# Optimization experiments

Hardware: AMD Instinct MI355X
Metric: run time of the kernel (lower is better)

The kernel has to match this reference:

```python
import jax, jax.numpy as jnp
import numpy as np

EMBED = 1024
HEADS = 16

def setup_inputs() -> dict:
    key = jax.random.key(0)
    ks = jax.random.split(key, 6)
    N, S = 1, 4096
    half = EMBED // 2
    x = jax.random.normal(ks[0], (N, S, EMBED), dtype=jnp.float32)
    Wq = jax.random.normal(ks[1], (half, half), dtype=jnp.float32) * 0.02
    Wk = jax.random.normal(ks[2], (half, half), dtype=jnp.float32) * 0.02
    Wv = jax.random.normal(ks[3], (half, half), dtype=jnp.float32) * 0.02
    Wo = jax.random.normal(ks[4], (EMBED, half), dtype=jnp.float32) * 0.02
    bo = jnp.zeros((EMBED,), dtype=jnp.float32)
    return {"x": x, "Wq": Wq, "Wk": Wk, "Wv": Wv, "Wo": Wo, "bo": bo}

def reference(x, Wq, Wk, Wv, Wo, bo):
    N, S, E = x.shape
    H = HEADS
    Dh = (E // 2) // H                 # per-head dim of the half-width projections (32)
    scale = float(E // H) ** 0.5       # original scales by head_dim = embed/heads = 64
    left = x[..., : E // 2]            # only the left chunk feeds attention in the source
    # torch Linear: y = x @ W.T (no bias)
    q = (left @ Wq.T).reshape(N, S, H, Dh)
    k = (left @ Wk.T).reshape(N, S, H, Dh)
    v = (left @ Wv.T).reshape(N, S, H, Dh)
    energy = jnp.einsum('nqhd,nkhd->nqkh', q, k)          # [N,S,S,H] full score tensor
    att = jax.nn.softmax(energy / scale, axis=2)          # softmax over key axis
    out = jnp.einsum('nqkh,nkhd->nqhd', att, v)           # [N,S,H,Dh]
    out = out.reshape(N, S, E // 2)
    return out @ Wo.T + bo                                # fc_out: half -> embed
```

## Files before the change

### kernel.cpp

```cpp
#include <hip/hip_runtime.h>
#include <stdint.h>


#define SEQ    4096
#define DMODEL 1024
#define DHALF  512
#define NH     16
#define DH     32
#define NSPLIT 2
#define KSPAN  (SEQ / NSPLIT)

typedef __attribute__((ext_vector_type(4))) float facc4;
typedef __attribute__((ext_vector_type(8))) short bfrag8;

#define MFMA_BF16(a, b, c) __builtin_amdgcn_mfma_f32_16x16x32_bf16((a), (b), (c), 0, 0, 0)

static __device__ __forceinline__ uint16_t f2b(float x) {
    uint32_t u = __float_as_uint(x);
    return (uint16_t)((u + 0x7FFFu + ((u >> 16) & 1u)) >> 16);
}
static __device__ __forceinline__ float b2f(uint16_t b) {
    return __uint_as_float(((uint32_t)b) << 16);
}

static __device__ __forceinline__ bfrag8 cvt8(const float* __restrict__ s) {
    float4 a = *(const float4*)s;
    float4 b = *(const float4*)(s + 4);
    bfrag8 r;
    r[0] = (short)f2b(a.x); r[1] = (short)f2b(a.y);
    r[2] = (short)f2b(a.z); r[3] = (short)f2b(a.w);
    r[4] = (short)f2b(b.x); r[5] = (short)f2b(b.y);
    r[6] = (short)f2b(b.z); r[7] = (short)f2b(b.w);
    return r;
}

__global__ __launch_bounds__(256) void convert_all(
    const float* __restrict__ x,  const float* __restrict__ Wq,
    const float* __restrict__ Wk, const float* __restrict__ Wv,
    const float* __restrict__ Wo,
    uint16_t* __restrict__ xbf, uint16_t* __restrict__ Wqb,
    uint16_t* __restrict__ Wkb, uint16_t* __restrict__ Wvb,
    uint16_t* __restrict__ Wob)
{
    int bid = blockIdx.x;
    if (bid < 1024) {
        int t   = bid * 256 + threadIdx.x;
        int row = t >> 6;
        int cb  = (t & 63) << 3;
        *(bfrag8*)&xbf[(size_t)row * DHALF + cb] = cvt8(&x[(size_t)row * DMODEL + cb]);
    } else {
        int zz = bid - 1024;
        const float* src; uint16_t* dst; size_t off;
        if      (zz < 128) { src = Wq; dst = Wqb; off = (size_t)zz * 2048; }
        else if (zz < 256) { src = Wk; dst = Wkb; off = (size_t)(zz - 128) * 2048; }
        else if (zz < 384) { src = Wv; dst = Wvb; off = (size_t)(zz - 256) * 2048; }
        else               { src = Wo; dst = Wob; off = (size_t)(zz - 384) * 2048; }
        size_t i = off + (size_t)threadIdx.x * 8;
        *(bfrag8*)&dst[i] = cvt8(&src[i]);
    }
}

__device__ __forceinline__ void gemm128(
    const uint16_t* __restrict__ A, int lda,
    const uint16_t* __restrict__ B, int ldb,
    void* __restrict__ C, int ldc, int cF32,
    const float* __restrict__ bias, float scale,
    int Kd, int m0, int n0)
{
    __shared__ __align__(16) uint16_t As[2][128 * 40];
    __shared__ __align__(16) uint16_t Bs[2][128 * 40];

    const int tid  = threadIdx.x;
    const int lane = tid & 63;
    const int wv   = tid >> 6;
    const int lo   = lane & 15;
    const int quad = lane >> 4;
    const int srow = tid >> 2;
    const int skq  = (tid & 3) * 8;
    const int rb   = (wv >> 1) * 64;
    const int cb   = (wv & 1) * 64;

    const facc4 ZACC = {0.f, 0.f, 0.f, 0.f};
    facc4 acc[4][4];
#pragma unroll
    for (int i = 0; i < 4; ++i)
#pragma unroll
        for (int j = 0; j < 4; ++j) acc[i][j] = ZACC;

    const uint16_t* pA0 = &A[(size_t)(m0 + srow) * lda + skq];
    const uint16_t* pA1 = &A[(size_t)(m0 + srow + 64) * lda + skq];
    const uint16_t* pB0 = &B[(size_t)(n0 + srow) * ldb + skq];
    const uint16_t* pB1 = &B[(size_t)(n0 + srow + 64) * ldb + skq];

    bfrag8 ra0 = *(const bfrag8*)pA0;
    bfrag8 ra1 = *(const bfrag8*)pA1;
    bfrag8 rb0 = *(const bfrag8*)pB0;
    bfrag8 rb1 = *(const bfrag8*)pB1;

    *(bfrag8*)&As[0][srow * 40 + skq]        = ra0;
    *(bfrag8*)&As[0][(srow + 64) * 40 + skq] = ra1;
    *(bfrag8*)&Bs[0][srow * 40 + skq]        = rb0;
    *(bfrag8*)&Bs[0][(srow + 64) * 40 + skq] = rb1;
    __syncthreads();

    int p = 0;
    for (int kt = 0; kt < Kd; kt += 32) {
        const bool more = (kt + 32 < Kd);
        if (more) {
            ra0 = *(const bfrag8*)(pA0 + kt + 32);
            ra1 = *(const bfrag8*)(pA1 + kt + 32);
            rb0 = *(const bfrag8*)(pB0 + kt + 32);
            rb1 = *(const bfrag8*)(pB1 + kt + 32);
        }

        bfrag8 af[4], bf[4];
#pragma unroll
        for (int i = 0; i < 4; ++i) {
            af[i] = *(const bfrag8*)&As[p][(rb + i * 16 + lo) * 40 + quad * 8];
            bf[i] = *(const bfrag8*)&Bs[p][(cb + i * 16 + lo) * 40 + quad * 8];
        }
#pragma unroll
        for (int i = 0; i < 4; ++i)
#pragma unroll
            for (int j = 0; j < 4; ++j)
                acc[i][j] = MFMA_BF16(af[i], bf[j], acc[i][j]);

        if (more) {
            *(bfrag8*)&As[1 - p][srow * 40 + skq]        = ra0;
            *(bfrag8*)&As[1 - p][(srow + 64) * 40 + skq] = ra1;
            *(bfrag8*)&Bs[1 - p][srow * 40 + skq]        = rb0;
            *(bfrag8*)&Bs[1 - p][(srow + 64) * 40 + skq] = rb1;
            __syncthreads();
            p ^= 1;
        }
    }

#pragma unroll
    for (int j = 0; j < 4; ++j) {
        int col  = n0 + cb + j * 16 + lo;
        float bv = bias ? bias[col] : 0.f;
#pragma unroll
        for (int i = 0; i < 4; ++i) {
#pragma unroll
            for (int r = 0; r < 4; ++r) {
                int row = m0 + rb + i * 16 + quad * 4 + r;
                float v = acc[i][j][r] * scale + bv;
                if (cF32) ((float*)C)[(size_t)row * ldc + col] = v;
                else      ((uint16_t*)C)[(size_t)row * ldc + col] = f2b(v);
            }
        }
    }
}

#define SC_Q (0.125f * 1.4426950408889634f)

__global__ __launch_bounds__(256, 2) void qkv_kernel(
    const uint16_t* __restrict__ xbf,
    const uint16_t* __restrict__ Wqb, const uint16_t* __restrict__ Wkb,
    const uint16_t* __restrict__ Wvb,
    uint16_t* __restrict__ Q, uint16_t* __restrict__ K, uint16_t* __restrict__ V)
{
    const int z = blockIdx.z;
    const uint16_t* W = (z == 0) ? Wqb : (z == 1) ? Wkb : Wvb;
    uint16_t* Out     = (z == 0) ? Q   : (z == 1) ? K   : V;
    float scale       = (z == 0) ? SC_Q : 1.0f;
    gemm128(xbf, DHALF, W, DHALF, Out, DHALF, 0, nullptr, scale, DHALF,
            blockIdx.y * 128, blockIdx.x * 128);
}

__global__ __launch_bounds__(256, 2) void outproj_kernel(
    const uint16_t* __restrict__ O, const uint16_t* __restrict__ Wob,
    const float* __restrict__ bo, float* __restrict__ Y)
{
    gemm128(O, DHALF, Wob, DHALF, Y, DMODEL, 1, bo, 1.0f, DHALF,
            blockIdx.y * 128, blockIdx.x * 128);
}

__global__ __launch_bounds__(256) void attn_kernel(
    const uint16_t* __restrict__ Q, const uint16_t* __restrict__ Kb,
    const uint16_t* __restrict__ Vb, uint16_t* __restrict__ Op,
    float* __restrict__ lbuf)
{
    __shared__ __align__(16) uint16_t Ks[2][64 * 40];
    __shared__ __align__(16) uint16_t Vt[2][32 * 64];
    __shared__ __align__(16) uint16_t Ps[4 * 16 * 72];

    const int tid  = threadIdx.x;
    const int lane = tid & 63;
    const int wv   = tid >> 6;
    const int lo   = lane & 15;
    const int quad = lane >> 4;
    const int h    = blockIdx.y;
    const int q0   = blockIdx.x * 64;
    const int sp   = blockIdx.z;
    const int srow = tid >> 2;
    const int skq  = (tid & 3) * 8;

    const facc4 ZACC = {0.f, 0.f, 0.f, 0.f};

    const bfrag8 qf = *(const bfrag8*)&Q[(size_t)(q0 + wv * 16 + lo) * DHALF + h * DH + quad * 8];

    int vt_w[8];
#pragma unroll
    for (int j = 0; j < 8; ++j) {
        int d  = skq + j;
        int Rd = ((d & 7) + 2 * (d >> 3)) & 7;
        vt_w[j] = d * 64 + ((((srow >> 3) + Rd) & 7) << 3) + (srow & 7);
    }
    int vt_r[2][2];
#pragma unroll
    for (int dt = 0; dt < 2; ++dt) {
        int d  = dt * 16 + lo;
        int Rd = ((d & 7) + 2 * (d >> 3)) & 7;
#pragma unroll
        for (int c = 0; c < 2; ++c)
            vt_r[c][dt] = d * 64 + ((((c * 4 + quad) + Rd) & 7) << 3);
    }
    const int pbase = wv * (16 * 72);
    const int ps_w  = pbase + lo * 72 + 4 * quad;
    const int ps_r  = pbase + lo * 72 + quad * 8;
    const int ks_r  = lo * 40 + quad * 8;

    const uint16_t* pK = &Kb[(size_t)srow * DHALF + h * DH + skq];
    const uint16_t* pV = &Vb[(size_t)srow * DHALF + h * DH + skq];

    facc4 oacc[2];
    oacc[0] = ZACC; oacc[1] = ZACC;
    float lpart = 0.f;

    const int kb0  = sp * KSPAN;
    const int kend = kb0 + KSPAN;

    float4 kreg = *(const float4*)(pK + (size_t)kb0 * DHALF);
    float4 vreg = *(const float4*)(pV + (size_t)kb0 * DHALF);

    *(float4*)&Ks[0][srow * 40 + skq] = kreg;
    {
        const uint16_t* vp = (const uint16_t*)&vreg;
#pragma unroll
        for (int j = 0; j < 8; ++j) Vt[0][vt_w[j]] = vp[j];
    }
    __syncthreads();

    int p = 0;
    for (int kb = kb0; kb < kend; kb += 64) {
        const bool more = (kb + 64 < kend);
        if (more) {
            kreg = *(const float4*)(pK + (size_t)(kb + 64) * DHALF);
            vreg = *(const float4*)(pV + (size_t)(kb + 64) * DHALF);
        }

#pragma unroll
        for (int t = 0; t < 4; ++t) {
            bfrag8 kf = *(const bfrag8*)&Ks[p][t * 640 + ks_r];
            facc4 s = MFMA_BF16(kf, qf, ZACC);
            float p0 = __builtin_amdgcn_exp2f(s[0]);
            float p1 = __builtin_amdgcn_exp2f(s[1]);
            float p2 = __builtin_amdgcn_exp2f(s[2]);
            float p3 = __builtin_amdgcn_exp2f(s[3]);
            lpart += (p0 + p1) + (p2 + p3);
            uint32_t u0 = __float_as_uint(p0) + 0x8000u;
            uint32_t u1 = __float_as_uint(p1) + 0x8000u;
            uint32_t u2 = __float_as_uint(p2) + 0x8000u;
            uint32_t u3 = __float_as_uint(p3) + 0x8000u;
            uint2 w;
            w.x = __builtin_amdgcn_perm(u1, u0, 0x07060302u);
            w.y = __builtin_amdgcn_perm(u3, u2, 0x07060302u);
            *(uint2*)&Ps[ps_w + 16 * t] = w;
        }
        __builtin_amdgcn_wave_barrier();

#pragma unroll
        for (int c = 0; c < 2; ++c) {
            bfrag8 pf = *(const bfrag8*)&Ps[ps_r + c * 32];
#pragma unroll
            for (int dt = 0; dt < 2; ++dt) {
                bfrag8 vf = *(const bfrag8*)&Vt[p][vt_r[c][dt]];
                oacc[dt] = MFMA_BF16(pf, vf, oacc[dt]);
            }
        }

        if (more) {
            *(float4*)&Ks[1 - p][srow * 40 + skq] = kreg;
            const uint16_t* vp = (const uint16_t*)&vreg;
#pragma unroll
            for (int j = 0; j < 8; ++j) Vt[1 - p][vt_w[j]] = vp[j];
            __syncthreads();
            p ^= 1;
        }
    }

    float lfull = lpart;
    lfull += __shfl_xor(lfull, 16);
    lfull += __shfl_xor(lfull, 32);
    if (quad == 0)
        lbuf[((size_t)sp * NH + h) * SEQ + q0 + wv * 16 + lo] = lfull;

    uint16_t* Od = Op + (size_t)sp * SEQ * DHALF;
#pragma unroll
    for (int r = 0; r < 4; ++r) {
        int row = q0 + wv * 16 + quad * 4 + r;
        Od[(size_t)row * DHALF + h * DH + lo]      = f2b(oacc[0][r]);
        Od[(size_t)row * DHALF + h * DH + 16 + lo] = f2b(oacc[1][r]);
    }
}

__global__ __launch_bounds__(256) void combine_kernel(
    const uint16_t* __restrict__ Op, const float* __restrict__ lbuf,
    uint16_t* __restrict__ O)
{
    int t   = blockIdx.x * 256 + threadIdx.x;
    int row = t >> 6;
    int cb  = (t & 63) << 3;
    int h   = cb >> 5;
    float inv = 1.0f / (lbuf[(size_t)h * SEQ + row] +
                        lbuf[((size_t)NH + h) * SEQ + row]);
    const uint16_t* p0 = &Op[(size_t)row * DHALF + cb];
    const uint16_t* p1 = p0 + (size_t)SEQ * DHALF;
    bfrag8 a = *(const bfrag8*)p0;
    bfrag8 b = *(const bfrag8*)p1;
    bfrag8 o;
#pragma unroll
    for (int j = 0; j < 8; ++j)
        o[j] = (short)f2b((b2f((uint16_t)a[j]) + b2f((uint16_t)b[j])) * inv);
    *(bfrag8*)&O[(size_t)row * DHALF + cb] = o;
}

extern "C" void kernel_launch(void* const* d_in, const int* in_sizes, int n_in,
                              void* d_out, int out_size, void* d_ws, size_t ws_size,
                              hipStream_t stream)
{
    const float* x  = (const float*)d_in[0];
    const float* Wq = (const float*)d_in[1];
    const float* Wk = (const float*)d_in[2];
    const float* Wv = (const float*)d_in[3];
    const float* Wo = (const float*)d_in[4];
    const float* bo = (const float*)d_in[5];

    uint16_t* xbf = (uint16_t*)d_ws;
    uint16_t* Wqb = xbf + (size_t)SEQ * DHALF;
    uint16_t* Wkb = Wqb + (size_t)DHALF * DHALF;
    uint16_t* Wvb = Wkb + (size_t)DHALF * DHALF;
    uint16_t* Wob = Wvb + (size_t)DHALF * DHALF;
    uint16_t* Q   = Wob + (size_t)DMODEL * DHALF;
    uint16_t* K   = Q + (size_t)SEQ * DHALF;
    uint16_t* V   = K + (size_t)SEQ * DHALF;
    uint16_t* O   = V + (size_t)SEQ * DHALF;
    uint16_t* Op  = O + (size_t)SEQ * DHALF;
    float*  lbuf  = (float*)(Op + (size_t)NSPLIT * SEQ * DHALF);

    convert_all<<<1664, 256, 0, stream>>>(x, Wq, Wk, Wv, Wo, xbf, Wqb, Wkb, Wvb, Wob);
    qkv_kernel<<<dim3(DHALF / 128, SEQ / 128, 3), 256, 0, stream>>>(
        xbf, Wqb, Wkb, Wvb, Q, K, V);
    attn_kernel<<<dim3(SEQ / 64, NH, NSPLIT), 256, 0, stream>>>(Q, K, V, Op, lbuf);
    combine_kernel<<<1024, 256, 0, stream>>>(Op, lbuf, O);
    outproj_kernel<<<dim3(DMODEL / 128, SEQ / 128), 256, 0, stream>>>(
        O, Wob, bo, (float*)d_out);
}
```

Baseline: 197.7 us.

## Split attention keys across waves and keep P in registers via K16 MFMA

```diff
diff --git a/kernel.cpp b/kernel.cpp
--- a/kernel.cpp
+++ b/kernel.cpp
@@ -12,8 +12,10 @@
 
 typedef __attribute__((ext_vector_type(4))) float facc4;
 typedef __attribute__((ext_vector_type(8))) short bfrag8;
-
-#define MFMA_BF16(a, b, c) __builtin_amdgcn_mfma_f32_16x16x32_bf16((a), (b), (c), 0, 0, 0)
+typedef __attribute__((ext_vector_type(4))) short bpack4;
+
+#define MFMA_BF16(a, b, c)  __builtin_amdgcn_mfma_f32_16x16x32_bf16((a), (b), (c), 0, 0, 0)
+#define MFMA_BF16_K16(a, b, c) __builtin_amdgcn_mfma_f32_16x16x16bf16_1k((a), (b), (c), 0, 0, 0)
 
 static __device__ __forceinline__ uint16_t f2b(float x) {
     uint32_t u = __float_as_uint(x);
@@ -181,9 +183,9 @@
     const uint16_t* __restrict__ Vb, uint16_t* __restrict__ Op,
     float* __restrict__ lbuf)
 {
-    __shared__ __align__(16) uint16_t Ks[2][64 * 40];
     __shared__ __align__(16) uint16_t Vt[2][32 * 64];
-    __shared__ __align__(16) uint16_t Ps[4 * 16 * 72];
+    __shared__ float Ored[64][33];
+    __shared__ float lsh[4][64];
 
     const int tid  = threadIdx.x;
     const int lane = tid & 63;
@@ -198,7 +200,10 @@
 
     const facc4 ZACC = {0.f, 0.f, 0.f, 0.f};
 
-    const bfrag8 qf = *(const bfrag8*)&Q[(size_t)(q0 + wv * 16 + lo) * DHALF + h * DH + quad * 8];
+    bfrag8 qf[4];
+#pragma unroll
+    for (int t = 0; t < 4; ++t)
+        qf[t] = *(const bfrag8*)&Q[(size_t)(q0 + t * 16 + lo) * DHALF + h * DH + quad * 8];
 
     int vt_w[8];
 #pragma unroll
@@ -207,34 +212,28 @@
         int Rd = ((d & 7) + 2 * (d >> 3)) & 7;
         vt_w[j] = d * 64 + ((((srow >> 3) + Rd) & 7) << 3) + (srow & 7);
     }
-    int vt_r[2][2];
+    int vt_r[2];
 #pragma unroll
     for (int dt = 0; dt < 2; ++dt) {
         int d  = dt * 16 + lo;
         int Rd = ((d & 7) + 2 * (d >> 3)) & 7;
-#pragma unroll
-        for (int c = 0; c < 2; ++c)
-            vt_r[c][dt] = d * 64 + ((((c * 4 + quad) + Rd) & 7) << 3);
-    }
-    const int pbase = wv * (16 * 72);
-    const int ps_w  = pbase + lo * 72 + 4 * quad;
-    const int ps_r  = pbase + lo * 72 + quad * 8;
-    const int ks_r  = lo * 40 + quad * 8;
-
-    const uint16_t* pK = &Kb[(size_t)srow * DHALF + h * DH + skq];
+        vt_r[dt] = d * 64 + ((((2 * wv + (quad >> 1)) + Rd) & 7) << 3) + (quad & 1) * 4;
+    }
+
+    const uint16_t* pK = &Kb[(size_t)(wv * 16 + lo) * DHALF + h * DH + quad * 8];
     const uint16_t* pV = &Vb[(size_t)srow * DHALF + h * DH + skq];
 
-    facc4 oacc[2];
-    oacc[0] = ZACC; oacc[1] = ZACC;
-    float lpart = 0.f;
+    facc4 oacc[4][2];
+#pragma unroll
+    for (int t = 0; t < 4; ++t) { oacc[t][0] = ZACC; oacc[t][1] = ZACC; }
+    float lp[4] = {0.f, 0.f, 0.f, 0.f};
 
     const int kb0  = sp * KSPAN;
     const int kend = kb0 + KSPAN;
 
-    float4 kreg = *(const float4*)(pK + (size_t)kb0 * DHALF);
+    bfrag8 kf   = *(const bfrag8*)(pK + (size_t)kb0 * DHALF);
     float4 vreg = *(const float4*)(pV + (size_t)kb0 * DHALF);
 
-    *(float4*)&Ks[0][srow * 40 + skq] = kreg;
     {
         const uint16_t* vp = (const uint16_t*)&vreg;
 #pragma unroll
@@ -245,20 +244,24 @@
     int p = 0;
     for (int kb = kb0; kb < kend; kb += 64) {
         const bool more = (kb + 64 < kend);
+        bfrag8 kf2;
         if (more) {
-            kreg = *(const float4*)(pK + (size_t)(kb + 64) * DHALF);
+            kf2  = *(const bfrag8*)(pK + (size_t)(kb + 64) * DHALF);
             vreg = *(const float4*)(pV + (size_t)(kb + 64) * DHALF);
         }
 
+        bpack4 vf[2];
+        vf[0] = *(const bpack4*)&Vt[p][vt_r[0]];
+        vf[1] = *(const bpack4*)&Vt[p][vt_r[1]];
+
 #pragma unroll
         for (int t = 0; t < 4; ++t) {
-            bfrag8 kf = *(const bfrag8*)&Ks[p][t * 640 + ks_r];
-            facc4 s = MFMA_BF16(kf, qf, ZACC);
+            facc4 s = MFMA_BF16(kf, qf[t], ZACC);
             float p0 = __builtin_amdgcn_exp2f(s[0]);
             float p1 = __builtin_amdgcn_exp2f(s[1]);
             float p2 = __builtin_amdgcn_exp2f(s[2]);
             float p3 = __builtin_amdgcn_exp2f(s[3]);
-            lpart += (p0 + p1) + (p2 + p3);
+            lp[t] += (p0 + p1) + (p2 + p3);
             uint32_t u0 = __float_as_uint(p0) + 0x8000u;
             uint32_t u1 = __float_as_uint(p1) + 0x8000u;
             uint32_t u2 = __float_as_uint(p2) + 0x8000u;
@@ -266,42 +269,58 @@
             uint2 w;
             w.x = __builtin_amdgcn_perm(u1, u0, 0x07060302u);
             w.y = __builtin_amdgcn_perm(u3, u2, 0x07060302u);
-            *(uint2*)&Ps[ps_w + 16 * t] = w;
-        }
-        __builtin_amdgcn_wave_barrier();
-
-#pragma unroll
-        for (int c = 0; c < 2; ++c) {
-            bfrag8 pf = *(const bfrag8*)&Ps[ps_r + c * 32];
-#pragma unroll
-            for (int dt = 0; dt < 2; ++dt) {
-                bfrag8 vf = *(const bfrag8*)&Vt[p][vt_r[c][dt]];
-                oacc[dt] = MFMA_BF16(pf, vf, oacc[dt]);
-            }
+            bpack4 pf = *(bpack4*)&w;
+#pragma unroll
+            for (int dt = 0; dt < 2; ++dt)
+                oacc[t][dt] = MFMA_BF16_K16(pf, vf[dt], oacc[t][dt]);
         }
 
         if (more) {
-            *(float4*)&Ks[1 - p][srow * 40 + skq] = kreg;
             const uint16_t* vp = (const uint16_t*)&vreg;
 #pragma unroll
             for (int j = 0; j < 8; ++j) Vt[1 - p][vt_w[j]] = vp[j];
+            kf = kf2;
             __syncthreads();
             p ^= 1;
         }
     }
 
-    float lfull = lpart;
-    lfull += __shfl_xor(lfull, 16);
-    lfull += __shfl_xor(lfull, 32);
-    if (quad == 0)
-        lbuf[((size_t)sp * NH + h) * SEQ + q0 + wv * 16 + lo] = lfull;
-
-    uint16_t* Od = Op + (size_t)sp * SEQ * DHALF;
-#pragma unroll
-    for (int r = 0; r < 4; ++r) {
-        int row = q0 + wv * 16 + quad * 4 + r;
-        Od[(size_t)row * DHALF + h * DH + lo]      = f2b(oacc[0][r]);
-        Od[(size_t)row * DHALF + h * DH + 16 + lo] = f2b(oacc[1][r]);
+#pragma unroll
+    for (int t = 0; t < 4; ++t) {
+        float l = lp[t];
+        l += __shfl_xor(l, 16);
+        l += __shfl_xor(l, 32);
+        if (quad == 0) lsh[wv][t * 16 + lo] = l;
+    }
+
+    for (int w = 0; w < 4; ++w) {
+        if (wv == w) {
+#pragma unroll
+            for (int t = 0; t < 4; ++t)
+#pragma unroll
+                for (int dt = 0; dt < 2; ++dt)
+#pragma unroll
+                    for (int r = 0; r < 4; ++r) {
+                        int q = t * 16 + quad * 4 + r;
+                        int d = dt * 16 + lo;
+                        if (w == 0) Ored[q][d]  = oacc[t][dt][r];
+                        else        Ored[q][d] += oacc[t][dt][r];
+                    }
+        }
+        __syncthreads();
+    }
+
+    {
+        int row = tid >> 2;
+        int dc  = (tid & 3) * 8;
+        bfrag8 o8;
+#pragma unroll
+        for (int j = 0; j < 8; ++j) o8[j] = (short)f2b(Ored[row][dc + j]);
+        uint16_t* Od = Op + (size_t)sp * SEQ * DHALF;
+        *(bfrag8*)&Od[(size_t)(q0 + row) * DHALF + h * DH + dc] = o8;
+        if (tid < 64)
+            lbuf[((size_t)sp * NH + h) * SEQ + q0 + tid] =
+                lsh[0][tid] + lsh[1][tid] + lsh[2][tid] + lsh[3][tid];
     }
 }
 
```

Result: slower. 213.6 us (+8.0%).

## Fuse x conversion into QKV GEMM, single-buffer attention, compute rowsum via MFMA

Applied to the files above, without the earlier changes.

```diff
diff --git a/kernel.cpp b/kernel.cpp
--- a/kernel.cpp
+++ b/kernel.cpp
@@ -7,8 +7,6 @@
 #define DHALF  512
 #define NH     16
 #define DH     32
-#define NSPLIT 2
-#define KSPAN  (SEQ / NSPLIT)
 
 typedef __attribute__((ext_vector_type(4))) float facc4;
 typedef __attribute__((ext_vector_type(8))) short bfrag8;
@@ -23,45 +21,40 @@
     return __uint_as_float(((uint32_t)b) << 16);
 }
 
-static __device__ __forceinline__ bfrag8 cvt8(const float* __restrict__ s) {
-    float4 a = *(const float4*)s;
-    float4 b = *(const float4*)(s + 4);
-    bfrag8 r;
-    r[0] = (short)f2b(a.x); r[1] = (short)f2b(a.y);
-    r[2] = (short)f2b(a.z); r[3] = (short)f2b(a.w);
-    r[4] = (short)f2b(b.x); r[5] = (short)f2b(b.y);
-    r[6] = (short)f2b(b.z); r[7] = (short)f2b(b.w);
-    return r;
-}
-
-__global__ __launch_bounds__(256) void convert_all(
-    const float* __restrict__ x,  const float* __restrict__ Wq,
-    const float* __restrict__ Wk, const float* __restrict__ Wv,
-    const float* __restrict__ Wo,
-    uint16_t* __restrict__ xbf, uint16_t* __restrict__ Wqb,
-    uint16_t* __restrict__ Wkb, uint16_t* __restrict__ Wvb,
-    uint16_t* __restrict__ Wob)
-{
-    int bid = blockIdx.x;
-    if (bid < 1024) {
-        int t   = bid * 256 + threadIdx.x;
-        int row = t >> 6;
-        int cb  = (t & 63) << 3;
-        *(bfrag8*)&xbf[(size_t)row * DHALF + cb] = cvt8(&x[(size_t)row * DMODEL + cb]);
-    } else {
-        int zz = bid - 1024;
-        const float* src; uint16_t* dst; size_t off;
-        if      (zz < 128) { src = Wq; dst = Wqb; off = (size_t)zz * 2048; }
-        else if (zz < 256) { src = Wk; dst = Wkb; off = (size_t)(zz - 128) * 2048; }
-        else if (zz < 384) { src = Wv; dst = Wvb; off = (size_t)(zz - 256) * 2048; }
-        else               { src = Wo; dst = Wob; off = (size_t)(zz - 384) * 2048; }
-        size_t i = off + (size_t)threadIdx.x * 8;
-        *(bfrag8*)&dst[i] = cvt8(&src[i]);
-    }
-}
-
-__device__ __forceinline__ void gemm128(
-    const uint16_t* __restrict__ A, int lda,
+static __device__ __forceinline__ bfrag8 cvt8perm(float4 a, float4 b) {
+    uint32_t u0 = __float_as_uint(a.x) + 0x8000u, u1 = __float_as_uint(a.y) + 0x8000u;
+    uint32_t u2 = __float_as_uint(a.z) + 0x8000u, u3 = __float_as_uint(a.w) + 0x8000u;
+    uint32_t u4 = __float_as_uint(b.x) + 0x8000u, u5 = __float_as_uint(b.y) + 0x8000u;
+    uint32_t u6 = __float_as_uint(b.z) + 0x8000u, u7 = __float_as_uint(b.w) + 0x8000u;
+    union { uint32_t w[4]; bfrag8 r; } u;
+    u.w[0] = __builtin_amdgcn_perm(u1, u0, 0x07060302u);
+    u.w[1] = __builtin_amdgcn_perm(u3, u2, 0x07060302u);
+    u.w[2] = __builtin_amdgcn_perm(u5, u4, 0x07060302u);
+    u.w[3] = __builtin_amdgcn_perm(u7, u6, 0x07060302u);
+    return u.r;
+}
+
+__global__ __launch_bounds__(256) void convert_w(
+    const float* __restrict__ Wq, const float* __restrict__ Wk,
+    const float* __restrict__ Wv, const float* __restrict__ Wo,
+    uint16_t* __restrict__ q, uint16_t* __restrict__ k,
+    uint16_t* __restrict__ v, uint16_t* __restrict__ o)
+{
+    int zz = blockIdx.x;
+    const float* src; uint16_t* dst; size_t off;
+    if      (zz < 128) { src = Wq; dst = q; off = (size_t)zz * 2048; }
+    else if (zz < 256) { src = Wk; dst = k; off = (size_t)(zz - 128) * 2048; }
+    else if (zz < 384) { src = Wv; dst = v; off = (size_t)(zz - 256) * 2048; }
+    else               { src = Wo; dst = o; off = (size_t)(zz - 384) * 2048; }
+    size_t i = off + (size_t)threadIdx.x * 8;
+    float4 a = *(const float4*)&src[i];
+    float4 b = *(const float4*)&src[i + 4];
+    *(bfrag8*)&dst[i] = cvt8perm(a, b);
+}
+
+template <int AF32>
+__device__ __forceinline__ void gemm128T(
+    const void* __restrict__ A, int lda,
     const uint16_t* __restrict__ B, int ldb,
     void* __restrict__ C, int ldc, int cF32,
     const float* __restrict__ bias, float scale,
@@ -87,18 +80,32 @@
 #pragma unroll
         for (int j = 0; j < 4; ++j) acc[i][j] = ZACC;
 
-    const uint16_t* pA0 = &A[(size_t)(m0 + srow) * lda + skq];
-    const uint16_t* pA1 = &A[(size_t)(m0 + srow + 64) * lda + skq];
+    const float*    fA0 = AF32 ? &((const float*)A)[(size_t)(m0 + srow) * lda + skq] : nullptr;
+    const float*    fA1 = AF32 ? &((const float*)A)[(size_t)(m0 + srow + 64) * lda + skq] : nullptr;
+    const uint16_t* hA0 = AF32 ? nullptr : &((const uint16_t*)A)[(size_t)(m0 + srow) * lda + skq];
+    const uint16_t* hA1 = AF32 ? nullptr : &((const uint16_t*)A)[(size_t)(m0 + srow + 64) * lda + skq];
     const uint16_t* pB0 = &B[(size_t)(n0 + srow) * ldb + skq];
     const uint16_t* pB1 = &B[(size_t)(n0 + srow + 64) * ldb + skq];
 
-    bfrag8 ra0 = *(const bfrag8*)pA0;
-    bfrag8 ra1 = *(const bfrag8*)pA1;
+    bfrag8 ra0, ra1;
+    float4 f0a, f0b, f1a, f1b;
+    if (AF32) {
+        f0a = *(const float4*)fA0; f0b = *(const float4*)(fA0 + 4);
+        f1a = *(const float4*)fA1; f1b = *(const float4*)(fA1 + 4);
+    } else {
+        ra0 = *(const bfrag8*)hA0;
+        ra1 = *(const bfrag8*)hA1;
+    }
     bfrag8 rb0 = *(const bfrag8*)pB0;
     bfrag8 rb1 = *(const bfrag8*)pB1;
 
-    *(bfrag8*)&As[0][srow * 40 + skq]        = ra0;
-    *(bfrag8*)&As[0][(srow + 64) * 40 + skq] = ra1;
+    if (AF32) {
+        *(bfrag8*)&As[0][srow * 40 + skq]        = cvt8perm(f0a, f0b);
+        *(bfrag8*)&As[0][(srow + 64) * 40 + skq] = cvt8perm(f1a, f1b);
+    } else {
+        *(bfrag8*)&As[0][srow * 40 + skq]        = ra0;
+        *(bfrag8*)&As[0][(srow + 64) * 40 + skq] = ra1;
+    }
     *(bfrag8*)&Bs[0][srow * 40 + skq]        = rb0;
     *(bfrag8*)&Bs[0][(srow + 64) * 40 + skq] = rb1;
     __syncthreads();
@@ -107,8 +114,13 @@
     for (int kt = 0; kt < Kd; kt += 32) {
         const bool more = (kt + 32 < Kd);
         if (more) {
-            ra0 = *(const bfrag8*)(pA0 + kt + 32);
-            ra1 = *(const bfrag8*)(pA1 + kt + 32);
+            if (AF32) {
+                f0a = *(const float4*)(fA0 + kt + 32); f0b = *(const float4*)(fA0 + kt + 36);
+                f1a = *(const float4*)(fA1 + kt + 32); f1b = *(const float4*)(fA1 + kt + 36);
+            } else {
+                ra0 = *(const bfrag8*)(hA0 + kt + 32);
+                ra1 = *(const bfrag8*)(hA1 + kt + 32);
+            }
             rb0 = *(const bfrag8*)(pB0 + kt + 32);
             rb1 = *(const bfrag8*)(pB1 + kt + 32);
         }
@@ -126,8 +138,13 @@
                 acc[i][j] = MFMA_BF16(af[i], bf[j], acc[i][j]);
 
         if (more) {
-            *(bfrag8*)&As[1 - p][srow * 40 + skq]        = ra0;
-            *(bfrag8*)&As[1 - p][(srow + 64) * 40 + skq] = ra1;
+            if (AF32) {
+                *(bfrag8*)&As[1 - p][srow * 40 + skq]        = cvt8perm(f0a, f0b);
+                *(bfrag8*)&As[1 - p][(srow + 64) * 40 + skq] = cvt8perm(f1a, f1b);
+            } else {
+                *(bfrag8*)&As[1 - p][srow * 40 + skq]        = ra0;
+                *(bfrag8*)&As[1 - p][(srow + 64) * 40 + skq] = ra1;
+            }
             *(bfrag8*)&Bs[1 - p][srow * 40 + skq]        = rb0;
             *(bfrag8*)&Bs[1 - p][(srow + 64) * 40 + skq] = rb1;
             __syncthreads();
@@ -155,7 +172,7 @@
 #define SC_Q (0.125f * 1.4426950408889634f)
 
 __global__ __launch_bounds__(256, 2) void qkv_kernel(
-    const uint16_t* __restrict__ xbf,
+    const float* __restrict__ x,
     const uint16_t* __restrict__ Wqb, const uint16_t* __restrict__ Wkb,
     const uint16_t* __restrict__ Wvb,
     uint16_t* __restrict__ Q, uint16_t* __restrict__ K, uint16_t* __restrict__ V)
@@ -164,25 +181,25 @@
     const uint16_t* W = (z == 0) ? Wqb : (z == 1) ? Wkb : Wvb;
     uint16_t* Out     = (z == 0) ? Q   : (z == 1) ? K   : V;
     float scale       = (z == 0) ? SC_Q : 1.0f;
-    gemm128(xbf, DHALF, W, DHALF, Out, DHALF, 0, nullptr, scale, DHALF,
-            blockIdx.y * 128, blockIdx.x * 128);
+    gemm128T<1>(x, DMODEL, W, DHALF, Out, DHALF, 0, nullptr, scale, DHALF,
+                blockIdx.y * 128, blockIdx.x * 128);
 }
 
 __global__ __launch_bounds__(256, 2) void outproj_kernel(
     const uint16_t* __restrict__ O, const uint16_t* __restrict__ Wob,
     const float* __restrict__ bo, float* __restrict__ Y)
 {
-    gemm128(O, DHALF, Wob, DHALF, Y, DMODEL, 1, bo, 1.0f, DHALF,
-            blockIdx.y * 128, blockIdx.x * 128);
+    gemm128T<0>(O, DHALF, Wob, DHALF, Y, DMODEL, 1, bo, 1.0f, DHALF,
+                blockIdx.y * 128, blockIdx.x * 128);
 }
 
 __global__ __launch_bounds__(256) void attn_kernel(
     const uint16_t* __restrict__ Q, const uint16_t* __restrict__ Kb,
     const uint16_t* __restrict__ Vb, uint16_t* __restrict__ Op,
-    float* __restrict__ lbuf)
-{
-    __shared__ __align__(16) uint16_t Ks[2][64 * 40];
-    __shared__ __align__(16) uint16_t Vt[2][32 * 64];
+    float* __restrict__ lbuf, int kspan)
+{
+    __shared__ __align__(16) uint16_t Ks[64 * 40];
+    __shared__ __align__(16) uint16_t Vt[32 * 64];
     __shared__ __align__(16) uint16_t Ps[4 * 16 * 72];
 
     const int tid  = threadIdx.x;
@@ -200,6 +217,10 @@
 
     const bfrag8 qf = *(const bfrag8*)&Q[(size_t)(q0 + wv * 16 + lo) * DHALF + h * DH + quad * 8];
 
+    bfrag8 ones;
+#pragma unroll
+    for (int j = 0; j < 8; ++j) ones[j] = (short)0x3F80;
+
     int vt_w[8];
 #pragma unroll
     for (int j = 0; j < 8; ++j) {
@@ -224,41 +245,37 @@
     const uint16_t* pK = &Kb[(size_t)srow * DHALF + h * DH + skq];
     const uint16_t* pV = &Vb[(size_t)srow * DHALF + h * DH + skq];
 
-    facc4 oacc[2];
-    oacc[0] = ZACC; oacc[1] = ZACC;
-    float lpart = 0.f;
-
-    const int kb0  = sp * KSPAN;
-    const int kend = kb0 + KSPAN;
+    facc4 oacc[2], oaccL;
+    oacc[0] = ZACC; oacc[1] = ZACC; oaccL = ZACC;
+
+    const int kb0  = sp * kspan;
+    const int kend = kb0 + kspan;
 
     float4 kreg = *(const float4*)(pK + (size_t)kb0 * DHALF);
     float4 vreg = *(const float4*)(pV + (size_t)kb0 * DHALF);
 
-    *(float4*)&Ks[0][srow * 40 + skq] = kreg;
-    {
-        const uint16_t* vp = (const uint16_t*)&vreg;
-#pragma unroll
-        for (int j = 0; j < 8; ++j) Vt[0][vt_w[j]] = vp[j];
-    }
-    __syncthreads();
-
-    int p = 0;
     for (int kb = kb0; kb < kend; kb += 64) {
-        const bool more = (kb + 64 < kend);
-        if (more) {
+        *(float4*)&Ks[srow * 40 + skq] = kreg;
+        {
+            const uint16_t* vp = (const uint16_t*)&vreg;
+#pragma unroll
+            for (int j = 0; j < 8; ++j) Vt[vt_w[j]] = vp[j];
+        }
+        __syncthreads();
+
+        if (kb + 64 < kend) {
             kreg = *(const float4*)(pK + (size_t)(kb + 64) * DHALF);
             vreg = *(const float4*)(pV + (size_t)(kb + 64) * DHALF);
         }
 
 #pragma unroll
         for (int t = 0; t < 4; ++t) {
-            bfrag8 kf = *(const bfrag8*)&Ks[p][t * 640 + ks_r];
+            bfrag8 kf = *(const bfrag8*)&Ks[t * 640 + ks_r];
             facc4 s = MFMA_BF16(kf, qf, ZACC);
             float p0 = __builtin_amdgcn_exp2f(s[0]);
             float p1 = __builtin_amdgcn_exp2f(s[1]);
             float p2 = __builtin_amdgcn_exp2f(s[2]);
             float p3 = __builtin_amdgcn_exp2f(s[3]);
-            lpart += (p0 + p1) + (p2 + p3);
             uint32_t u0 = __float_as_uint(p0) + 0x8000u;
             uint32_t u1 = __float_as_uint(p1) + 0x8000u;
             uint32_t u2 = __float_as_uint(p2) + 0x8000u;
@@ -275,26 +292,19 @@
             bfrag8 pf = *(const bfrag8*)&Ps[ps_r + c * 32];
 #pragma unroll
             for (int dt = 0; dt < 2; ++dt) {
-                bfrag8 vf = *(const bfrag8*)&Vt[p][vt_r[c][dt]];
+                bfrag8 vf = *(const bfrag8*)&Vt[vt_r[c][dt]];
                 oacc[dt] = MFMA_BF16(pf, vf, oacc[dt]);
             }
-        }
-
-        if (more) {
-            *(float4*)&Ks[1 - p][srow * 40 + skq] = kreg;
-            const uint16_t* vp = (const uint16_t*)&vreg;
-#pragma unroll
-            for (int j = 0; j < 8; ++j) Vt[1 - p][vt_w[j]] = vp[j];
-            __syncthreads();
-            p ^= 1;
-        }
-    }
-
-    float lfull = lpart;
-    lfull += __shfl_xor(lfull, 16);
-    lfull += __shfl_xor(lfull, 32);
-    if (quad == 0)
-        lbuf[((size_t)sp * NH + h) * SEQ + q0 + wv * 16 + lo] = lfull;
+            oaccL = MFMA_BF16(pf, ones, oaccL);
+        }
+        __syncthreads();
+    }
+
+    if (lo == 0) {
+#pragma unroll
+        for (int r = 0; r < 4; ++r)
+            lbuf[((size_t)sp * NH + h) * SEQ + q0 + wv * 16 + quad * 4 + r] = oaccL[r];
+    }
 
     uint16_t* Od = Op + (size_t)sp * SEQ * DHALF;
 #pragma unroll
@@ -307,22 +317,24 @@
 
 __global__ __launch_bounds__(256) void combine_kernel(
     const uint16_t* __restrict__ Op, const float* __restrict__ lbuf,
-    uint16_t* __restrict__ O)
+    uint16_t* __restrict__ O, int ns)
 {
     int t   = blockIdx.x * 256 + threadIdx.x;
     int row = t >> 6;
     int cb  = (t & 63) << 3;
     int h   = cb >> 5;
-    float inv = 1.0f / (lbuf[(size_t)h * SEQ + row] +
-                        lbuf[((size_t)NH + h) * SEQ + row]);
-    const uint16_t* p0 = &Op[(size_t)row * DHALF + cb];
-    const uint16_t* p1 = p0 + (size_t)SEQ * DHALF;
-    bfrag8 a = *(const bfrag8*)p0;
-    bfrag8 b = *(const bfrag8*)p1;
+    float l = 0.f;
+    float acc[8] = {0.f, 0.f, 0.f, 0.f, 0.f, 0.f, 0.f, 0.f};
+    for (int sp = 0; sp < ns; ++sp) {
+        l += lbuf[((size_t)sp * NH + h) * SEQ + row];
+        bfrag8 a = *(const bfrag8*)&Op[(size_t)sp * SEQ * DHALF + (size_t)row * DHALF + cb];
+#pragma unroll
+        for (int j = 0; j < 8; ++j) acc[j] += b2f((uint16_t)a[j]);
+    }
+    float inv = 1.0f / l;
     bfrag8 o;
 #pragma unroll
-    for (int j = 0; j < 8; ++j)
-        o[j] = (short)f2b((b2f((uint16_t)a[j]) + b2f((uint16_t)b[j])) * inv);
+    for (int j = 0; j < 8; ++j) o[j] = (short)f2b(acc[j] * inv);
     *(bfrag8*)&O[(size_t)row * DHALF + cb] = o;
 }
 
@@ -337,8 +349,13 @@
     const float* Wo = (const float*)d_in[4];
     const float* bo = (const float*)d_in[5];
 
-    uint16_t* xbf = (uint16_t*)d_ws;
-    uint16_t* Wqb = xbf + (size_t)SEQ * DHALF;
+    size_t fixed_e = 3 * (size_t)DHALF * DHALF + (size_t)DMODEL * DHALF
+                   + 4 * (size_t)SEQ * DHALF;
+    size_t need4 = (fixed_e + 4 * (size_t)SEQ * DHALF) * 2
+                 + 4 * (size_t)NH * SEQ * 4;
+    const int ns = (ws_size >= need4) ? 4 : 2;
+
+    uint16_t* Wqb = (uint16_t*)d_ws;
     uint16_t* Wkb = Wqb + (size_t)DHALF * DHALF;
     uint16_t* Wvb = Wkb + (size_t)DHALF * DHALF;
     uint16_t* Wob = Wvb + (size_t)DHALF * DHALF;
@@ -347,13 +364,13 @@
     uint16_t* V   = K + (size_t)SEQ * DHALF;
     uint16_t* O   = V + (size_t)SEQ * DHALF;
     uint16_t* Op  = O + (size_t)SEQ * DHALF;
-    float*  lbuf  = (float*)(Op + (size_t)NSPLIT * SEQ * DHALF);
-
-    convert_all<<<1664, 256, 0, stream>>>(x, Wq, Wk, Wv, Wo, xbf, Wqb, Wkb, Wvb, Wob);
+    float*  lbuf  = (float*)(Op + (size_t)ns * SEQ * DHALF);
+
+    convert_w<<<640, 256, 0, stream>>>(Wq, Wk, Wv, Wo, Wqb, Wkb, Wvb, Wob);
     qkv_kernel<<<dim3(DHALF / 128, SEQ / 128, 3), 256, 0, stream>>>(
-        xbf, Wqb, Wkb, Wvb, Q, K, V);
-    attn_kernel<<<dim3(SEQ / 64, NH, NSPLIT), 256, 0, stream>>>(Q, K, V, Op, lbuf);
-    combine_kernel<<<1024, 256, 0, stream>>>(Op, lbuf, O);
+        x, Wqb, Wkb, Wvb, Q, K, V);
+    attn_kernel<<<dim3(SEQ / 64, NH, ns), 256, 0, stream>>>(Q, K, V, Op, lbuf, SEQ / ns);
+    combine_kernel<<<1024, 256, 0, stream>>>(Op, lbuf, O, ns);
     outproj_kernel<<<dim3(DMODEL / 128, SEQ / 128), 256, 0, stream>>>(
         O, Wob, bo, (float*)d_out);
 }
```

New measurement: 194.5 us. No clear change (-1.6%).
